# Optimization experiments

Hardware: AMD Instinct MI355X
Metric: run time of the kernel (lower is better)

Reference implementation:

```python
import jax, jax.numpy as jnp
import numpy as np

N = 50000
E = 800000
IN_C, HID_C, OUT_C = 128, 128, 64


def setup_inputs() -> dict:
    key = jax.random.key(0)
    ks = jax.random.split(key, 12)
    x = jax.random.normal(ks[0], (N, IN_C), dtype=jnp.float32)
    edge_index = jax.random.randint(ks[1], (2, E), 0, N, dtype=jnp.int64)
    dims = [(IN_C, HID_C), (HID_C, HID_C), (HID_C, OUT_C)]
    params = {}
    for i, (din, dout) in enumerate(dims):
        s = 1.0 / np.sqrt(din)
        params[f"Wl{i}"] = jax.random.uniform(ks[2 + 3 * i], (din, dout), jnp.float32, -s, s)
        params[f"b{i}"] = jnp.zeros((dout,), jnp.float32)
        params[f"Wr{i}"] = jax.random.uniform(ks[3 + 3 * i], (din, dout), jnp.float32, -s, s)
    return {"x": x, "edge_index": edge_index, **params}


def _sage_conv(x, src, dst, Wl, b, Wr):
    # mean-aggregate neighbor features: messages flow src -> dst
    agg = jax.ops.segment_sum(x[src], dst, num_segments=N)          # [N, d]
    deg = jax.ops.segment_sum(jnp.ones((src.shape[0],), x.dtype), dst, num_segments=N)
    agg = agg / jnp.maximum(deg, 1.0)[:, None]                      # mean (0 for isolated nodes)
    return agg @ Wl + b + x @ Wr


def reference(x, edge_index, Wl0, b0, Wr0, Wl1, b1, Wr1, Wl2, b2, Wr2):
    src, dst = edge_index[0], edge_index[1]
    h = _sage_conv(x, src, dst, Wl0, b0, Wr0)
    h = jax.nn.relu(h)  # dropout is identity in eval mode
    h = _sage_conv(h, src, dst, Wl1, b1, Wr1)
    h = jax.nn.relu(h)
    h = _sage_conv(h, src, dst, Wl2, b2, Wr2)
    return h
```

## Files before the change

### kernel.cpp

```cpp
#include <hip/hip_runtime.h>

#define N_NODES 50000
#define N_EDGES 800000
#define NBUCK 196
#define NPART 391
#define CELLCAP 36
#define BCAPN (NPART * CELLCAP)

typedef __attribute__((ext_vector_type(8))) short short8;
typedef __attribute__((ext_vector_type(4))) float f32x4;
typedef __attribute__((ext_vector_type(8))) unsigned short ushort8v;
typedef __attribute__((ext_vector_type(16))) unsigned char uchar16;


__device__ inline void split_bf16(float f, unsigned short& hi, unsigned short& lo) {
    union { float f; unsigned u; } a; a.f = f;
    unsigned r = (a.u + 0x7fffu + ((a.u >> 16) & 1u)) >> 16;
    hi = (unsigned short)r;
    union { unsigned u; float f; } b; b.u = r << 16;
    union { float f; unsigned u; } c; c.f = f - b.f;
    unsigned r2 = (c.u + 0x7fffu + ((c.u >> 16) & 1u)) >> 16;
    lo = (unsigned short)r2;
}

__device__ inline unsigned short f2bf(float f) {
    union { float f; unsigned u; } a; a.f = f;
    return (unsigned short)((a.u + 0x7fffu + ((a.u >> 16) & 1u)) >> 16);
}

__device__ inline float bf2f(unsigned short u) {
    union { unsigned u; float f; } a; a.u = (unsigned)u << 16; return a.f;
}

__device__ inline unsigned char q8(float v, float qs) {
    int qi = (int)rintf(v * qs);
    qi = qi > 127 ? 127 : (qi < -127 ? -127 : qi);
    return (unsigned char)(qi + 128);
}

__device__ inline void acc8(float* a, uint2 w, float s) {
#pragma unroll
    for (int j = 0; j < 4; ++j) {
        a[j]     += (float)((w.x >> (8 * j)) & 255u) * s;
        a[j + 4] += (float)((w.y >> (8 * j)) & 255u) * s;
    }
}


__global__ __launch_bounds__(256) void prep_part_kernel(
    const float* __restrict__ W0, const float* __restrict__ W1,
    const float* __restrict__ W2, const float* __restrict__ W3,
    const float* __restrict__ W4, const float* __restrict__ W5,
    unsigned short* __restrict__ wout,
    const float* __restrict__ x,
    unsigned char* __restrict__ xq, float* __restrict__ xsc,
    const int* __restrict__ src, const int* __restrict__ dst,
    unsigned int* __restrict__ ebuf, int* __restrict__ cellcnt) {
    __shared__ int hist[NBUCK], binoff[NBUCK], bincur[NBUCK];
    __shared__ int scanbuf[256];
    __shared__ unsigned int sortbuf[2048];
    const int vb = blockIdx.x, tid = threadIdx.x;
    if (vb < 320) {
        int t = vb * 256 + tid;
        const float* W; int D, local, half; size_t base;
        if (t < 65536) {
            int mat = t >> 14; local = t & 16383; D = 128; half = 16384;
            base = (size_t)mat * 32768;
            W = mat == 0 ? W0 : mat == 1 ? W1 : mat == 2 ? W2 : W3;
        } else {
            int m = (t - 65536) >> 13; local = (t - 65536) & 8191; D = 64; half = 8192;
            base = 131072 + (size_t)m * 16384;
            W = m == 0 ? W4 : W5;
        }
        int j = local & 7, lane = (local >> 3) & 63, ks = (local >> 9) & 3, ct = local >> 11;
        int k = ks * 32 + ((lane >> 4) << 3) + j;
        int n = (ct << 4) + (lane & 15);
        unsigned short hi, lo;
        split_bf16(W[k * D + n], hi, lo);
        wout[base + local] = hi;
        wout[base + half + local] = lo;
    } else if (vb < 1883) {
        int t = (vb - 320) * 256 + tid;
        if (t >= N_NODES * 8) return;
        const float* p = x + (size_t)t * 16;
        float4 v0 = *(const float4*)(p);
        float4 v1 = *(const float4*)(p + 4);
        float4 v2 = *(const float4*)(p + 8);
        float4 v3 = *(const float4*)(p + 12);
        float vv[16] = {v0.x, v0.y, v0.z, v0.w, v1.x, v1.y, v1.z, v1.w,
                        v2.x, v2.y, v2.z, v2.w, v3.x, v3.y, v3.z, v3.w};
        float m = 0.f;
#pragma unroll
        for (int j = 0; j < 16; ++j) m = fmaxf(m, fabsf(vv[j]));
        m = fmaxf(m, __shfl_xor(m, 1));
        m = fmaxf(m, __shfl_xor(m, 2));
        m = fmaxf(m, __shfl_xor(m, 4));
        float qs = m > 0.f ? 127.0f / m : 0.0f;
        uchar16 qv;
#pragma unroll
        for (int j = 0; j < 16; ++j) qv[j] = q8(vv[j], qs);
        *(uchar16*)(xq + (size_t)t * 16) = qv;
        if ((t & 7) == 0) xsc[t >> 3] = m * (1.0f / 127.0f);
    } else {
        const int pb = vb - 1883;
        const int base = pb * 2048;
        if (tid < NBUCK) hist[tid] = 0;
        __syncthreads();
        int myb[8]; unsigned int myp[8];
#pragma unroll
        for (int i = 0; i < 8; ++i) {
            int e = base + i * 256 + tid;
            if (e < N_EDGES) {
                int d = dst[e], s = src[e];
                myb[i] = d >> 8;
                myp[i] = ((unsigned)d << 16) | (unsigned)s;
                atomicAdd(&hist[myb[i]], 1);
            } else myb[i] = -1;
        }
        __syncthreads();
        int v = (tid < NBUCK) ? hist[tid] : 0;
        scanbuf[tid] = v;
        __syncthreads();
        for (int off = 1; off < 256; off <<= 1) {
            int t = (tid >= off) ? scanbuf[tid - off] : 0;
            __syncthreads();
            scanbuf[tid] += t;
            __syncthreads();
        }
        if (tid < NBUCK) {
            binoff[tid] = scanbuf[tid] - v;
            bincur[tid] = 0;
        }
        __syncthreads();
#pragma unroll
        for (int i = 0; i < 8; ++i) {
            if (myb[i] >= 0) {
                int r = atomicAdd(&bincur[myb[i]], 1);
                sortbuf[binoff[myb[i]] + r] = myp[i];
            }
        }
        __syncthreads();
        int nloc = N_EDGES - base; if (nloc > 2048) nloc = 2048;
#pragma unroll
        for (int i = 0; i < 8; ++i) {
            int idx = i * 256 + tid;
            if (idx < nloc) {
                unsigned int p = sortbuf[idx];
                int b = p >> 24;
                int off = idx - binoff[b];
                if (off < CELLCAP)
                    ebuf[(size_t)b * BCAPN + pb * CELLCAP + off] = p;
            }
        }
        if (tid < NBUCK)
            cellcnt[tid * NPART + pb] = (hist[tid] < CELLCAP) ? hist[tid] : CELLCAP;
    }
}


__global__ __launch_bounds__(256) void fine_fill_kernel(
    const unsigned int* __restrict__ ebuf, const int* __restrict__ cellcnt,
    int* __restrict__ rowbeg, int* __restrict__ rowend,
    unsigned short* __restrict__ esrc, int n) {
    __shared__ int cnt[256], scanbuf[256], cur[256];
    const int b = blockIdx.x, tid = threadIdx.x;
    const int nbase = b << 8;
    cnt[tid] = 0;
    __syncthreads();
    const size_t lo = (size_t)b * BCAPN;
    for (int i = tid; i < NPART; i += 256) {
        int c = cellcnt[b * NPART + i];
        const unsigned int* cell = ebuf + lo + i * CELLCAP;
        for (int k = 0; k < c; ++k)
            atomicAdd(&cnt[(cell[k] >> 16) & 255], 1);
    }
    __syncthreads();
    int v = cnt[tid];
    scanbuf[tid] = v;
    __syncthreads();
    for (int off = 1; off < 256; off <<= 1) {
        int t = (tid >= off) ? scanbuf[tid - off] : 0;
        __syncthreads();
        scanbuf[tid] += t;
        __syncthreads();
    }
    int start = (int)lo + scanbuf[tid] - v;
    if (nbase + tid < n) { rowbeg[nbase + tid] = start; rowend[nbase + tid] = start + v; }
    cur[tid] = start;
    __syncthreads();
    for (int i = tid; i < NPART; i += 256) {
        int c = cellcnt[b * NPART + i];
        const unsigned int* cell = ebuf + lo + i * CELLCAP;
        for (int k = 0; k < c; ++k) {
            unsigned int p = cell[k];
            int pos = atomicAdd(&cur[(p >> 16) & 255], 1);
            esrc[pos] = (unsigned short)(p & 0xFFFFu);
        }
    }
}


template <int DOUT, bool RELU, bool QOUT>
__global__ __launch_bounds__(512, 6) void sage_layer(
    const unsigned char* __restrict__ Hq, const float* __restrict__ Hsc,
    const float* __restrict__ Hf,
    const int* __restrict__ rowbeg, const int* __restrict__ rowend,
    const unsigned short* __restrict__ esrc,
    const unsigned short* __restrict__ B1p, const unsigned short* __restrict__ B2p,
    const float* __restrict__ bias, float* __restrict__ outf,
    unsigned char* __restrict__ outq, float* __restrict__ outsc, int M) {
    constexpr int K = 128, BM = 32, KS = 4, CT = DOUT / 16;
    constexpr int PITCH = K + 8;
    constexpr int HALF = CT * KS * 512;
    constexpr bool SPLITRT = (CT == 4);
    constexpr int RTN = SPLITRT ? 1 : 2;
    __shared__ unsigned short As[3][BM * PITCH];
    __shared__ float wmax[BM][8];

    const int tid = threadIdx.x;
    const int r0 = blockIdx.x * BM;

    {
        int row = tid >> 4;
        int c8 = (tid & 15) * 8;
        int grow = r0 + row; if (grow >= M) grow = M - 1;
        const float* sp = Hf + (size_t)grow * K + c8;
        float4 v0 = *(const float4*)(sp);
        float4 v1 = *(const float4*)(sp + 4);
        float vv[8] = {v0.x, v0.y, v0.z, v0.w, v1.x, v1.y, v1.z, v1.w};
        ushort8v h, l;
#pragma unroll
        for (int j = 0; j < 8; ++j) {
            unsigned short a, b;
            split_bf16(vv[j], a, b);
            h[j] = a; l[j] = b;
        }
        *(ushort8v*)(&As[1][row * PITCH + c8]) = h;
        *(ushort8v*)(&As[2][row * PITCH + c8]) = l;
    }

    {
        const int g16 = tid >> 4, l16 = tid & 15;
        const unsigned char* __restrict__ Hb = Hq + l16 * 8;
        int node = r0 + g16; if (node >= M) node = M - 1;
        int beg = rowbeg[node], end = rowend[node];
        float a0[8] = {0,0,0,0,0,0,0,0}, a1[8] = {0,0,0,0,0,0,0,0};
        float sacc = 0.f;
        int k = beg;
        for (; k + 6 <= end; k += 6) {
            int e0 = esrc[k],     e1 = esrc[k + 1], e2 = esrc[k + 2];
            int e3 = esrc[k + 3], e4 = esrc[k + 4], e5 = esrc[k + 5];
            uint2 w0 = *(const uint2*)(Hb + (size_t)e0 * 128);
            uint2 w1 = *(const uint2*)(Hb + (size_t)e1 * 128);
            uint2 w2 = *(const uint2*)(Hb + (size_t)e2 * 128);
            uint2 w3 = *(const uint2*)(Hb + (size_t)e3 * 128);
            uint2 w4 = *(const uint2*)(Hb + (size_t)e4 * 128);
            uint2 w5 = *(const uint2*)(Hb + (size_t)e5 * 128);
            float s0 = Hsc[e0], s1 = Hsc[e1], s2 = Hsc[e2];
            float s3 = Hsc[e3], s4 = Hsc[e4], s5 = Hsc[e5];
            acc8(a0, w0, s0); acc8(a1, w1, s1); acc8(a0, w2, s2);
            acc8(a1, w3, s3); acc8(a0, w4, s4); acc8(a1, w5, s5);
            sacc += s0 + s1 + s2 + s3 + s4 + s5;
        }
        for (; k + 2 <= end; k += 2) {
            int e0 = esrc[k], e1 = esrc[k + 1];
            uint2 w0 = *(const uint2*)(Hb + (size_t)e0 * 128);
            uint2 w1 = *(const uint2*)(Hb + (size_t)e1 * 128);
            float s0 = Hsc[e0], s1 = Hsc[e1];
            acc8(a0, w0, s0); acc8(a1, w1, s1);
            sacc += s0 + s1;
        }
        if (k < end) {
            int e0 = esrc[k];
            uint2 w0 = *(const uint2*)(Hb + (size_t)e0 * 128);
            float s0 = Hsc[e0];
            acc8(a0, w0, s0);
            sacc += s0;
        }
        float inv = (end > beg) ? 1.0f / (float)(end - beg) : 0.0f;
        ushort8v mh;
#pragma unroll
        for (int j = 0; j < 8; ++j)
            mh[j] = f2bf((a0[j] + a1[j] - 128.0f * sacc) * inv);
        *(ushort8v*)(&As[0][g16 * PITCH + l16 * 8]) = mh;
    }
    __syncthreads();

    const int wave = tid >> 6, lane = tid & 63;
    const int rl = lane & 15, quad = lane >> 4;
    const int ct = SPLITRT ? (wave & 3) : wave;
    const int rt0 = SPLITRT ? (wave >> 2) : 0;

    f32x4 acc[RTN];
    {
        float bv = bias[ct * 16 + rl];
#pragma unroll
        for (int ri = 0; ri < RTN; ++ri) acc[ri] = (f32x4){bv, bv, bv, bv};
    }

#pragma unroll
    for (int ks = 0; ks < KS; ++ks) {
        short8 a_ag[RTN], a_sh[RTN][2];
#pragma unroll
        for (int ri = 0; ri < RTN; ++ri) {
            int rt = rt0 + ri;
            int off = (rt * 16 + rl) * PITCH + ks * 32 + quad * 8;
            a_ag[ri]    = *(const short8*)(&As[0][off]);
            a_sh[ri][0] = *(const short8*)(&As[1][off]);
            a_sh[ri][1] = *(const short8*)(&As[2][off]);
        }
        size_t boff = (((size_t)ct * KS + ks) * 64 + lane) * 8;
        short8 b1h = *(const short8*)(B1p + boff);
        short8 b1l = *(const short8*)(B1p + HALF + boff);
        short8 b2h = *(const short8*)(B2p + boff);
        short8 b2l = *(const short8*)(B2p + HALF + boff);
#pragma unroll
        for (int ri = 0; ri < RTN; ++ri) {
            acc[ri] = __builtin_amdgcn_mfma_f32_16x16x32_bf16(a_ag[ri],    b1h, acc[ri], 0, 0, 0);
            acc[ri] = __builtin_amdgcn_mfma_f32_16x16x32_bf16(a_ag[ri],    b1l, acc[ri], 0, 0, 0);
            acc[ri] = __builtin_amdgcn_mfma_f32_16x16x32_bf16(a_sh[ri][0], b2h, acc[ri], 0, 0, 0);
            acc[ri] = __builtin_amdgcn_mfma_f32_16x16x32_bf16(a_sh[ri][0], b2l, acc[ri], 0, 0, 0);
            acc[ri] = __builtin_amdgcn_mfma_f32_16x16x32_bf16(a_sh[ri][1], b2h, acc[ri], 0, 0, 0);
        }
    }

    if (RELU) {
#pragma unroll
        for (int ri = 0; ri < RTN; ++ri)
#pragma unroll
            for (int r = 0; r < 4; ++r)
                acc[ri][r] = fmaxf(acc[ri][r], 0.f);
    }

    float qsc[RTN][4];
    if constexpr (QOUT) {
        float lm[RTN][4];
#pragma unroll
        for (int ri = 0; ri < RTN; ++ri)
#pragma unroll
            for (int r = 0; r < 4; ++r) lm[ri][r] = fabsf(acc[ri][r]);
#pragma unroll
        for (int off = 1; off < 16; off <<= 1)
#pragma unroll
            for (int ri = 0; ri < RTN; ++ri)
#pragma unroll
                for (int r = 0; r < 4; ++r)
                    lm[ri][r] = fmaxf(lm[ri][r], __shfl_xor(lm[ri][r], off));
        if (rl == 0) {
#pragma unroll
            for (int ri = 0; ri < RTN; ++ri)
#pragma unroll
                for (int r = 0; r < 4; ++r)
                    wmax[(rt0 + ri) * 16 + quad * 4 + r][wave] = lm[ri][r];
        }
        __syncthreads();
#pragma unroll
        for (int ri = 0; ri < RTN; ++ri)
#pragma unroll
            for (int r = 0; r < 4; ++r) {
                int row = (rt0 + ri) * 16 + quad * 4 + r;
                float rm = fmaxf(fmaxf(fmaxf(wmax[row][0], wmax[row][1]),
                                       fmaxf(wmax[row][2], wmax[row][3])),
                                 fmaxf(fmaxf(wmax[row][4], wmax[row][5]),
                                       fmaxf(wmax[row][6], wmax[row][7])));
                qsc[ri][r] = rm > 0.f ? 127.0f / rm : 0.0f;
                if (wave == 0 && rl == 0) {
                    int rr = r0 + row;
                    if (rr < M) outsc[rr] = rm * (1.0f / 127.0f);
                }
            }
    }

#pragma unroll
    for (int ri = 0; ri < RTN; ++ri) {
        int rt = rt0 + ri;
        int col = ct * 16 + rl;
        int rowb = r0 + rt * 16 + quad * 4;
#pragma unroll
        for (int r = 0; r < 4; ++r) {
            int rr = rowb + r;
            if (rr < M) {
                float vv = acc[ri][r];
                outf[(size_t)rr * DOUT + col] = vv;
                if (QOUT) outq[(size_t)rr * DOUT + col] = q8(vv, qsc[ri][r]);
            }
        }
    }
}


extern "C" void kernel_launch(void* const* d_in, const int* in_sizes, int n_in,
                              void* d_out, int out_size, void* d_ws, size_t ws_size,
                              hipStream_t stream) {
    const float* x   = (const float*)d_in[0];
    const int* eidx  = (const int*)d_in[1];
    const int* src   = eidx;
    const int* dst   = eidx + N_EDGES;
    const float* Wl0 = (const float*)d_in[2];
    const float* b0  = (const float*)d_in[3];
    const float* Wr0 = (const float*)d_in[4];
    const float* Wl1 = (const float*)d_in[5];
    const float* b1  = (const float*)d_in[6];
    const float* Wr1 = (const float*)d_in[7];
    const float* Wl2 = (const float*)d_in[8];
    const float* b2  = (const float*)d_in[9];
    const float* Wr2 = (const float*)d_in[10];
    float* outp = (float*)d_out;

    float* hA = (float*)d_ws;
    float* hB = hA + (size_t)N_NODES * 128;
    unsigned int* ebuf = (unsigned int*)hA;
    unsigned char* xq = (unsigned char*)(hB + (size_t)N_NODES * 128);
    unsigned char* yq = xq + (size_t)N_NODES * 128;
    float* xsc = (float*)(yq + (size_t)N_NODES * 128);
    float* ysc = xsc + N_NODES;
    int* rowbeg = (int*)(ysc + N_NODES);
    int* rowend = rowbeg + N_NODES;
    int* cellcnt = rowend + N_NODES;
    unsigned short* esrc = (unsigned short*)(cellcnt + NBUCK * NPART);
    unsigned short* packw = esrc + (size_t)NBUCK * BCAPN;
    unsigned short* Wl0p = packw;
    unsigned short* Wr0p = packw + 32768;
    unsigned short* Wl1p = packw + 65536;
    unsigned short* Wr1p = packw + 98304;
    unsigned short* Wl2p = packw + 131072;
    unsigned short* Wr2p = packw + 147456;

    prep_part_kernel<<<1883 + NPART, 256, 0, stream>>>(
        Wl0, Wr0, Wl1, Wr1, Wl2, Wr2, packw, x, xq, xsc,
        src, dst, ebuf, cellcnt);
    fine_fill_kernel<<<NBUCK, 256, 0, stream>>>(ebuf, cellcnt, rowbeg, rowend, esrc, N_NODES);

    const int gemmGrid = (N_NODES + 31) / 32;

    sage_layer<128, true, true><<<gemmGrid, 512, 0, stream>>>(
        xq, xsc, x, rowbeg, rowend, esrc, Wl0p, Wr0p, b0,
        hA, yq, ysc, N_NODES);
    sage_layer<128, true, true><<<gemmGrid, 512, 0, stream>>>(
        yq, ysc, hA, rowbeg, rowend, esrc, Wl1p, Wr1p, b1,
        hB, xq, xsc, N_NODES);
    sage_layer<64, false, false><<<gemmGrid, 512, 0, stream>>>(
        xq, xsc, hB, rowbeg, rowend, esrc, Wl2p, Wr2p, b2,
        outp, nullptr, nullptr, N_NODES);
}
```

Baseline: 222.5 us.

## Fuse fine-fill into prep kernel using atomic completion counter spin-wait

Merges the fine_fill kernel into the prep/partition kernel by appending NBUCK extra blocks that spin on a global done counter until all partition blocks have published their cells with a release atomic. This removes one kernel launch and the inter-kernel gap, and lets fine-fill blocks start as soon as partitioning finishes while other prep blocks may still run. It adds a memset launch, relies on blocks being scheduled in index order to avoid deadlock, and spinning blocks occupy CU slots while they wait.

```diff
diff --git a/kernel.cpp b/kernel.cpp
--- a/kernel.cpp
+++ b/kernel.cpp
@@ -47,7 +47,7 @@
 }
 
 
-__global__ __launch_bounds__(256) void prep_part_kernel(
+__global__ __launch_bounds__(256) void prep_part_ff_kernel(
     const float* __restrict__ W0, const float* __restrict__ W1,
     const float* __restrict__ W2, const float* __restrict__ W3,
     const float* __restrict__ W4, const float* __restrict__ W5,
@@ -55,10 +55,10 @@
     const float* __restrict__ x,
     unsigned char* __restrict__ xq, float* __restrict__ xsc,
     const int* __restrict__ src, const int* __restrict__ dst,
-    unsigned int* __restrict__ ebuf, int* __restrict__ cellcnt) {
-    __shared__ int hist[NBUCK], binoff[NBUCK], bincur[NBUCK];
-    __shared__ int scanbuf[256];
-    __shared__ unsigned int sortbuf[2048];
+    unsigned int* __restrict__ ebuf, int* __restrict__ cellcnt,
+    int* __restrict__ rowbeg, int* __restrict__ rowend,
+    unsigned short* __restrict__ esrc, int* __restrict__ done) {
+    __shared__ __align__(16) unsigned char smem[12288];
     const int vb = blockIdx.x, tid = threadIdx.x;
     if (vb < 320) {
         int t = vb * 256 + tid;
@@ -101,7 +101,12 @@
         for (int j = 0; j < 16; ++j) qv[j] = q8(vv[j], qs);
         *(uchar16*)(xq + (size_t)t * 16) = qv;
         if ((t & 7) == 0) xsc[t >> 3] = m * (1.0f / 127.0f);
-    } else {
+    } else if (vb < 1883 + NPART) {
+        int* hist = (int*)smem;
+        int* binoff = hist + NBUCK;
+        int* bincur = binoff + NBUCK;
+        int* scanbuf = bincur + NBUCK;
+        unsigned int* sortbuf = (unsigned int*)(scanbuf + 256);
         const int pb = vb - 1883;
         const int base = pb * 2048;
         if (tid < NBUCK) hist[tid] = 0;
@@ -154,47 +159,53 @@
         }
         if (tid < NBUCK)
             cellcnt[tid * NPART + pb] = (hist[tid] < CELLCAP) ? hist[tid] : CELLCAP;
-    }
-}
-
-
-__global__ __launch_bounds__(256) void fine_fill_kernel(
-    const unsigned int* __restrict__ ebuf, const int* __restrict__ cellcnt,
-    int* __restrict__ rowbeg, int* __restrict__ rowend,
-    unsigned short* __restrict__ esrc, int n) {
-    __shared__ int cnt[256], scanbuf[256], cur[256];
-    const int b = blockIdx.x, tid = threadIdx.x;
-    const int nbase = b << 8;
-    cnt[tid] = 0;
-    __syncthreads();
-    const size_t lo = (size_t)b * BCAPN;
-    for (int i = tid; i < NPART; i += 256) {
-        int c = cellcnt[b * NPART + i];
-        const unsigned int* cell = ebuf + lo + i * CELLCAP;
-        for (int k = 0; k < c; ++k)
-            atomicAdd(&cnt[(cell[k] >> 16) & 255], 1);
-    }
-    __syncthreads();
-    int v = cnt[tid];
-    scanbuf[tid] = v;
-    __syncthreads();
-    for (int off = 1; off < 256; off <<= 1) {
-        int t = (tid >= off) ? scanbuf[tid - off] : 0;
-        __syncthreads();
-        scanbuf[tid] += t;
-        __syncthreads();
-    }
-    int start = (int)lo + scanbuf[tid] - v;
-    if (nbase + tid < n) { rowbeg[nbase + tid] = start; rowend[nbase + tid] = start + v; }
-    cur[tid] = start;
-    __syncthreads();
-    for (int i = tid; i < NPART; i += 256) {
-        int c = cellcnt[b * NPART + i];
-        const unsigned int* cell = ebuf + lo + i * CELLCAP;
-        for (int k = 0; k < c; ++k) {
-            unsigned int p = cell[k];
-            int pos = atomicAdd(&cur[(p >> 16) & 255], 1);
-            esrc[pos] = (unsigned short)(p & 0xFFFFu);
+        __threadfence();
+        __syncthreads();
+        if (tid == 0)
+            __hip_atomic_fetch_add(done, 1, __ATOMIC_RELEASE, __HIP_MEMORY_SCOPE_AGENT);
+    } else {
+        int* cnt = (int*)smem;
+        int* scanbuf = cnt + 256;
+        int* cur = scanbuf + 256;
+        const int b = vb - (1883 + NPART);
+        if (tid == 0) {
+            while (__hip_atomic_load(done, __ATOMIC_RELAXED, __HIP_MEMORY_SCOPE_AGENT) < NPART)
+                __builtin_amdgcn_s_sleep(32);
+            __hip_atomic_load(done, __ATOMIC_ACQUIRE, __HIP_MEMORY_SCOPE_AGENT);
+        }
+        __syncthreads();
+        const int nbase = b << 8;
+        cnt[tid] = 0;
+        __syncthreads();
+        const size_t lo = (size_t)b * BCAPN;
+        for (int i = tid; i < NPART; i += 256) {
+            int c = cellcnt[b * NPART + i];
+            const unsigned int* cell = ebuf + lo + i * CELLCAP;
+            for (int k = 0; k < c; ++k)
+                atomicAdd(&cnt[(cell[k] >> 16) & 255], 1);
+        }
+        __syncthreads();
+        int v = cnt[tid];
+        scanbuf[tid] = v;
+        __syncthreads();
+        for (int off = 1; off < 256; off <<= 1) {
+            int t = (tid >= off) ? scanbuf[tid - off] : 0;
+            __syncthreads();
+            scanbuf[tid] += t;
+            __syncthreads();
+        }
+        int start = (int)lo + scanbuf[tid] - v;
+        if (nbase + tid < N_NODES) { rowbeg[nbase + tid] = start; rowend[nbase + tid] = start + v; }
+        cur[tid] = start;
+        __syncthreads();
+        for (int i = tid; i < NPART; i += 256) {
+            int c = cellcnt[b * NPART + i];
+            const unsigned int* cell = ebuf + lo + i * CELLCAP;
+            for (int k = 0; k < c; ++k) {
+                unsigned int p = cell[k];
+                int pos = atomicAdd(&cur[(p >> 16) & 255], 1);
+                esrc[pos] = (unsigned short)(p & 0xFFFFu);
+            }
         }
     }
 }
@@ -417,7 +428,8 @@
     int* rowbeg = (int*)(ysc + N_NODES);
     int* rowend = rowbeg + N_NODES;
     int* cellcnt = rowend + N_NODES;
-    unsigned short* esrc = (unsigned short*)(cellcnt + NBUCK * NPART);
+    int* done = cellcnt + NBUCK * NPART;
+    unsigned short* esrc = (unsigned short*)(done + 16);
     unsigned short* packw = esrc + (size_t)NBUCK * BCAPN;
     unsigned short* Wl0p = packw;
     unsigned short* Wr0p = packw + 32768;
@@ -426,10 +438,10 @@
     unsigned short* Wl2p = packw + 131072;
     unsigned short* Wr2p = packw + 147456;
 
-    prep_part_kernel<<<1883 + NPART, 256, 0, stream>>>(
+    hipMemsetAsync(done, 0, sizeof(int), stream);
+    prep_part_ff_kernel<<<1883 + NPART + NBUCK, 256, 0, stream>>>(
         Wl0, Wr0, Wl1, Wr1, Wl2, Wr2, packw, x, xq, xsc,
-        src, dst, ebuf, cellcnt);
-    fine_fill_kernel<<<NBUCK, 256, 0, stream>>>(ebuf, cellcnt, rowbeg, rowend, esrc, N_NODES);
+        src, dst, ebuf, cellcnt, rowbeg, rowend, esrc, done);
 
     const int gemmGrid = (N_NODES + 31) / 32;
 
```

Result: slower. 297.9 us (+33.9%).

## Sort nodes by in-degree so each layer block processes similar-degree rows

Applied to the files above, without the earlier changes.

Builds a degree histogram in fine_fill and adds a counting-sort kernel that produces a permutation of nodes grouped by in-degree. Each sage_layer block then processes 32 nodes of similar degree through the permutation, which is meant to reduce divergence and load imbalance in the per-node gather loops. In exchange it adds a kernel launch, a memset, permutation lookups, and scattered output stores plus scattered self-feature reads, which costs locality.

```diff
diff --git a/kernel.cpp b/kernel.cpp
--- a/kernel.cpp
+++ b/kernel.cpp
@@ -6,6 +6,7 @@
 #define NPART 391
 #define CELLCAP 36
 #define BCAPN (NPART * CELLCAP)
+#define DBINS 64
 
 typedef __attribute__((ext_vector_type(8))) short short8;
 typedef __attribute__((ext_vector_type(4))) float f32x4;
@@ -161,11 +162,12 @@
 __global__ __launch_bounds__(256) void fine_fill_kernel(
     const unsigned int* __restrict__ ebuf, const int* __restrict__ cellcnt,
     int* __restrict__ rowbeg, int* __restrict__ rowend,
-    unsigned short* __restrict__ esrc, int n) {
-    __shared__ int cnt[256], scanbuf[256], cur[256];
+    unsigned short* __restrict__ esrc, int* __restrict__ gbins, int n) {
+    __shared__ int cnt[256], scanbuf[256], cur[256], lbins[DBINS];
     const int b = blockIdx.x, tid = threadIdx.x;
     const int nbase = b << 8;
     cnt[tid] = 0;
+    if (tid < DBINS) lbins[tid] = 0;
     __syncthreads();
     const size_t lo = (size_t)b * BCAPN;
     for (int i = tid; i < NPART; i += 256) {
@@ -176,6 +178,7 @@
     }
     __syncthreads();
     int v = cnt[tid];
+    if (nbase + tid < n) atomicAdd(&lbins[v > 63 ? 63 : v], 1);
     scanbuf[tid] = v;
     __syncthreads();
     for (int off = 1; off < 256; off <<= 1) {
@@ -197,13 +200,44 @@
             esrc[pos] = (unsigned short)(p & 0xFFFFu);
         }
     }
+    __syncthreads();
+    if (tid < DBINS && lbins[tid]) atomicAdd(&gbins[tid], lbins[tid]);
+}
+
+
+__global__ __launch_bounds__(256) void sort_kernel(
+    const int* __restrict__ rowbeg, const int* __restrict__ rowend,
+    const int* __restrict__ gbins, int* __restrict__ gcur,
+    int* __restrict__ perm, int n) {
+    __shared__ int lbins[DBINS], lpos[DBINS];
+    const int tid = threadIdx.x;
+    const int node = blockIdx.x * 256 + tid;
+    if (tid < DBINS) lbins[tid] = 0;
+    __syncthreads();
+    int deg = -1;
+    if (node < n) {
+        deg = rowend[node] - rowbeg[node];
+        if (deg > 63) deg = 63;
+        atomicAdd(&lbins[deg], 1);
+    }
+    __syncthreads();
+    if (tid < DBINS) {
+        int s = 0;
+        for (int i = 0; i < tid; ++i) s += gbins[i];
+        lpos[tid] = s + atomicAdd(&gcur[tid], lbins[tid]);
+    }
+    __syncthreads();
+    if (node < n) {
+        int p = atomicAdd(&lpos[deg], 1);
+        perm[p] = node;
+    }
 }
 
 
 template <int DOUT, bool RELU, bool QOUT>
 __global__ __launch_bounds__(512, 6) void sage_layer(
     const unsigned char* __restrict__ Hq, const float* __restrict__ Hsc,
-    const float* __restrict__ Hf,
+    const float* __restrict__ Hf, const int* __restrict__ perm,
     const int* __restrict__ rowbeg, const int* __restrict__ rowend,
     const unsigned short* __restrict__ esrc,
     const unsigned short* __restrict__ B1p, const unsigned short* __restrict__ B2p,
@@ -224,7 +258,8 @@
         int row = tid >> 4;
         int c8 = (tid & 15) * 8;
         int grow = r0 + row; if (grow >= M) grow = M - 1;
-        const float* sp = Hf + (size_t)grow * K + c8;
+        int node = perm[grow];
+        const float* sp = Hf + (size_t)node * K + c8;
         float4 v0 = *(const float4*)(sp);
         float4 v1 = *(const float4*)(sp + 4);
         float vv[8] = {v0.x, v0.y, v0.z, v0.w, v1.x, v1.y, v1.z, v1.w};
@@ -242,7 +277,8 @@
     {
         const int g16 = tid >> 4, l16 = tid & 15;
         const unsigned char* __restrict__ Hb = Hq + l16 * 8;
-        int node = r0 + g16; if (node >= M) node = M - 1;
+        int g = r0 + g16; if (g >= M) g = M - 1;
+        int node = perm[g];
         int beg = rowbeg[node], end = rowend[node];
         float a0[8] = {0,0,0,0,0,0,0,0}, a1[8] = {0,0,0,0,0,0,0,0};
         float sacc = 0.f;
@@ -366,7 +402,7 @@
                 qsc[ri][r] = rm > 0.f ? 127.0f / rm : 0.0f;
                 if (wave == 0 && rl == 0) {
                     int rr = r0 + row;
-                    if (rr < M) outsc[rr] = rm * (1.0f / 127.0f);
+                    if (rr < M) outsc[perm[rr]] = rm * (1.0f / 127.0f);
                 }
             }
     }
@@ -380,9 +416,10 @@
         for (int r = 0; r < 4; ++r) {
             int rr = rowb + r;
             if (rr < M) {
+                int orow = perm[rr];
                 float vv = acc[ri][r];
-                outf[(size_t)rr * DOUT + col] = vv;
-                if (QOUT) outq[(size_t)rr * DOUT + col] = q8(vv, qsc[ri][r]);
+                outf[(size_t)orow * DOUT + col] = vv;
+                if (QOUT) outq[(size_t)orow * DOUT + col] = q8(vv, qsc[ri][r]);
             }
         }
     }
@@ -416,7 +453,10 @@
     float* ysc = xsc + N_NODES;
     int* rowbeg = (int*)(ysc + N_NODES);
     int* rowend = rowbeg + N_NODES;
-    int* cellcnt = rowend + N_NODES;
+    int* perm   = rowend + N_NODES;
+    int* gbins  = perm + N_NODES;
+    int* gcur   = gbins + DBINS;
+    int* cellcnt = gcur + DBINS;
     unsigned short* esrc = (unsigned short*)(cellcnt + NBUCK * NPART);
     unsigned short* packw = esrc + (size_t)NBUCK * BCAPN;
     unsigned short* Wl0p = packw;
@@ -426,20 +466,22 @@
     unsigned short* Wl2p = packw + 131072;
     unsigned short* Wr2p = packw + 147456;
 
+    hipMemsetAsync(gbins, 0, 2 * DBINS * sizeof(int), stream);
     prep_part_kernel<<<1883 + NPART, 256, 0, stream>>>(
         Wl0, Wr0, Wl1, Wr1, Wl2, Wr2, packw, x, xq, xsc,
         src, dst, ebuf, cellcnt);
-    fine_fill_kernel<<<NBUCK, 256, 0, stream>>>(ebuf, cellcnt, rowbeg, rowend, esrc, N_NODES);
+    fine_fill_kernel<<<NBUCK, 256, 0, stream>>>(ebuf, cellcnt, rowbeg, rowend, esrc, gbins, N_NODES);
+    sort_kernel<<<(N_NODES + 255) / 256, 256, 0, stream>>>(rowbeg, rowend, gbins, gcur, perm, N_NODES);
 
     const int gemmGrid = (N_NODES + 31) / 32;
 
     sage_layer<128, true, true><<<gemmGrid, 512, 0, stream>>>(
-        xq, xsc, x, rowbeg, rowend, esrc, Wl0p, Wr0p, b0,
+        xq, xsc, x, perm, rowbeg, rowend, esrc, Wl0p, Wr0p, b0,
         hA, yq, ysc, N_NODES);
     sage_layer<128, true, true><<<gemmGrid, 512, 0, stream>>>(
-        yq, ysc, hA, rowbeg, rowend, esrc, Wl1p, Wr1p, b1,
+        yq, ysc, hA, perm, rowbeg, rowend, esrc, Wl1p, Wr1p, b1,
         hB, xq, xsc, N_NODES);
     sage_layer<64, false, false><<<gemmGrid, 512, 0, stream>>>(
-        xq, xsc, hB, rowbeg, rowend, esrc, Wl2p, Wr2p, b2,
+        xq, xsc, hB, perm, rowbeg, rowend, esrc, Wl2p, Wr2p, b2,
         outp, nullptr, nullptr, N_NODES);
 }
```

After: 235.0 us. +5.6%, slower.
